# Kernel optimization log

Hardware: AMD Instinct MI355X
Metric: run time of the kernel (lower is better)

## Reference

```python
import jax, jax.numpy as jnp
import numpy as np

B, D, O = 16384, 1024, 1024
NUM_TASKS = 2
E = 4  # experts per group (2 task groups + 1 shared group)


def setup_inputs() -> dict:
    key = jax.random.key(0)
    ks = jax.random.split(key, 7)
    x = jax.random.normal(ks[0], (B, D), dtype=jnp.float32)
    # Stacked expert params: groups g in {task0, task1, shared}, each with E experts.
    W = jax.random.normal(ks[1], (3, E, D, O), dtype=jnp.float32) * 0.02  # Linear weight (in,out layout)
    b = jax.random.normal(ks[2], (3, E, O), dtype=jnp.float32) * 0.02
    # Per-task gates over (E specific + E shared) = 8 experts.
    Wg = jax.random.normal(ks[3], (NUM_TASKS, D, 2 * E), dtype=jnp.float32) * 0.02
    bg = jax.random.normal(ks[4], (NUM_TASKS, 2 * E), dtype=jnp.float32) * 0.02
    # Shared gate over all 3*E = 12 experts (is_top=False).
    Wgs = jax.random.normal(ks[5], (D, 3 * E), dtype=jnp.float32) * 0.02
    bgs = jax.random.normal(ks[6], (3 * E,), dtype=jnp.float32) * 0.02
    return {"x": x, "W": W, "b": b, "Wg": Wg, "bg": bg, "Wgs": Wgs, "bgs": bgs}


def reference(x, W, b, Wg, bg, Wgs, bgs):
    # All 12 experts share the same input (single-input branch): one batched GEMM.
    # h: [3, B, E, O]  (dropout is identity in eval mode)
    h = jax.nn.relu(jnp.einsum('bd,gedo->gbeo', x, W) + b[:, None, :, :])
    # Per-task gates: [T, B, 2E]
    sel_t = jax.nn.softmax(jnp.einsum('bd,tdm->tbm', x, Wg) + bg[:, None, :], axis=-1)
    outs = []
    for t in range(NUM_TASKS):
        mat = jnp.concatenate([h[t], h[2]], axis=1)  # [B, 2E, O]
        outs.append(jnp.einsum('bmo,bm->bo', mat, sel_t[t]))
    # Shared gate over all experts (is_top=False): [B, 3E]
    sel_s = jax.nn.softmax(x @ Wgs + bgs, axis=-1)
    mat_all = jnp.concatenate([h[0], h[1], h[2]], axis=1)  # [B, 3E, O]
    outs.append(jnp.einsum('bmo,bm->bo', mat_all, sel_s))
    return tuple(outs)
```

## Files before the change

### kernel.cpp

```cpp
#include <hip/hip_runtime.h>

typedef unsigned short ushort_t;
typedef __attribute__((ext_vector_type(8))) short short8;
typedef __attribute__((ext_vector_type(4))) float floatx4;

#define B_ROWS 16384
#define BO 16777216
#define MC 4096

__device__ __forceinline__ ushort_t f2bf(float f){
  unsigned u = __float_as_uint(f);
  u += 0x7fffu + ((u >> 16) & 1u);
  return (ushort_t)(u >> 16);
}
__device__ __forceinline__ float bf2f(ushort_t u){
  return __uint_as_float(((unsigned)u) << 16);
}

__device__ __forceinline__ void gld_lds16(void* l, const void* g){
  __builtin_amdgcn_global_load_lds(
      (__attribute__((address_space(1))) void*)(g),
      (__attribute__((address_space(3))) void*)(l), 16, 0, 0);
}

__global__ void cvt_x(const float* __restrict__ x, ushort_t* __restrict__ xb){
  const int i = (blockIdx.x * 256 + threadIdx.x) * 4;
  const floatx4 v = *(const floatx4*)(x + i);
  ushort4 o;
  o.x = f2bf(v[0]); o.y = f2bf(v[1]); o.z = f2bf(v[2]); o.w = f2bf(v[3]);
  *(ushort4*)(xb + i) = o;
}

__global__ void cvt_wt(const float* __restrict__ W, ushort_t* __restrict__ wt){
  __shared__ float t[64][65];
  const int blk = blockIdx.x;
  const int ge = blk >> 8, dt = (blk >> 4) & 15, ot = blk & 15;
  const float* src = W + ((size_t)ge << 20) + (size_t)(dt * 64) * 1024 + ot * 64;
  const int c4 = (threadIdx.x & 15) * 4, r0 = threadIdx.x >> 4;
#pragma unroll
  for (int p = 0; p < 4; ++p){
    const int r = r0 + p * 16;
    const floatx4 v = *(const floatx4*)(src + (size_t)r * 1024 + c4);
    t[r][c4] = v[0]; t[r][c4+1] = v[1]; t[r][c4+2] = v[2]; t[r][c4+3] = v[3];
  }
  __syncthreads();
  ushort_t* dst = wt + ((size_t)ge << 20) + (size_t)(ot * 64) * 1024 + dt * 64;
  const int d4 = (threadIdx.x & 15) * 4, o0 = threadIdx.x >> 4;
#pragma unroll
  for (int p = 0; p < 4; ++p){
    const int o = o0 + p * 16;
    ushort4 ov;
    ov.x = f2bf(t[d4][o]);   ov.y = f2bf(t[d4+1][o]);
    ov.z = f2bf(t[d4+2][o]); ov.w = f2bf(t[d4+3][o]);
    *(ushort4*)(dst + (size_t)o * 1024 + d4) = ov;
  }
}

__global__ void cvt_wg(const float* __restrict__ Wg, const float* __restrict__ bg,
                       const float* __restrict__ Wgs, const float* __restrict__ bgs,
                       ushort_t* __restrict__ wgcat, float* __restrict__ biascat){
  const int m = blockIdx.x;
#pragma unroll
  for (int j = 0; j < 4; ++j){
    const int d = j * 256 + threadIdx.x;
    float v;
    if (m < 16)      v = Wg[((size_t)((m >> 3) * 1024 + d)) * 8 + (m & 7)];
    else if (m < 28) v = Wgs[(size_t)d * 12 + (m - 16)];
    else             v = 0.f;
    wgcat[m * 1024 + d] = f2bf(v);
  }
  if (threadIdx.x == 0){
    float bv;
    if (m < 16)      bv = bg[m];
    else if (m < 28) bv = bgs[m - 16];
    else             bv = -1e30f;
    biascat[m] = bv;
  }
}

__global__ __launch_bounds__(256) void gates_mfma(
    const ushort_t* __restrict__ xb, const ushort_t* __restrict__ wgcat,
    const float* __restrict__ biascat, float* __restrict__ selT)
{
  __shared__ __align__(16) char gsm[20480];
  const int tid = threadIdx.x;
  const int lane = tid & 63;
  const int w = tid >> 6;
  const int lr = lane & 15;
  const int brow = blockIdx.x * 128;

  const int sc = (((tid & 7) ^ ((tid >> 3) & 7)) << 4);
  const char* aS = (const char*)xb + (size_t)(brow + (tid >> 3)) * 2048 + sc;
  const char* bS = (const char*)wgcat + (size_t)(tid >> 3) * 2048 + sc;

  const int kx0 = (((lane >> 4) << 4)) ^ ((lane & 7) << 4);
  const int kx1 = (64 + ((lane >> 4) << 4)) ^ ((lane & 7) << 4);

  int aOff[2], bOff[2];
#pragma unroll
  for (int m = 0; m < 2; ++m) aOff[m] = (w * 32 + m * 16 + lr) * 128;
#pragma unroll
  for (int n = 0; n < 2; ++n) bOff[n] = 16384 + (n * 16 + lr) * 128;

  const floatx4 fz = {0.f, 0.f, 0.f, 0.f};
  floatx4 hacc[2][2];
#pragma unroll
  for (int m = 0; m < 2; ++m)
#pragma unroll
    for (int n = 0; n < 2; ++n) hacc[m][n] = fz;

  for (int kt = 0; kt < 16; ++kt){
    const size_t ko = (size_t)kt * 128;
#pragma unroll
    for (int j = 0; j < 4; ++j)
      gld_lds16(gsm + j * 4096 + w * 1024, aS + (size_t)j * 65536 + ko);
    gld_lds16(gsm + 16384 + w * 1024, bS + ko);
    __syncthreads();
    short8 av[2][2], bv[2][2];
#pragma unroll
    for (int m = 0; m < 2; ++m){
      av[m][0] = *(const short8*)(gsm + aOff[m] + kx0);
      av[m][1] = *(const short8*)(gsm + aOff[m] + kx1);
    }
#pragma unroll
    for (int n = 0; n < 2; ++n){
      bv[n][0] = *(const short8*)(gsm + bOff[n] + kx0);
      bv[n][1] = *(const short8*)(gsm + bOff[n] + kx1);
    }
#pragma unroll
    for (int m = 0; m < 2; ++m)
#pragma unroll
      for (int n = 0; n < 2; ++n){
        hacc[m][n] = __builtin_amdgcn_mfma_f32_16x16x32_bf16(av[m][0], bv[n][0], hacc[m][n], 0, 0, 0);
        hacc[m][n] = __builtin_amdgcn_mfma_f32_16x16x32_bf16(av[m][1], bv[n][1], hacc[m][n], 0, 0, 0);
      }
    __syncthreads();
  }

  const float bc0 = biascat[lr];
  const float bc1 = biascat[16 + lr];
#pragma unroll
  for (int m = 0; m < 2; ++m){
#pragma unroll
    for (int r = 0; r < 4; ++r){
      float l0 = hacc[m][0][r] + bc0;
      float l1 = hacc[m][1][r] + bc1;
      float mx0 = l0;
#pragma unroll
      for (int s = 1; s < 8; s <<= 1) mx0 = fmaxf(mx0, __shfl_xor(mx0, s, 64));
      float e0 = __expf(l0 - mx0);
      float s0 = e0;
#pragma unroll
      for (int s = 1; s < 8; s <<= 1) s0 += __shfl_xor(s0, s, 64);
      float mx1 = l1;
#pragma unroll
      for (int s = 1; s < 16; s <<= 1) mx1 = fmaxf(mx1, __shfl_xor(mx1, s, 64));
      float e1 = __expf(l1 - mx1);
      float s1 = e1;
#pragma unroll
      for (int s = 1; s < 16; s <<= 1) s1 += __shfl_xor(s1, s, 64);
      const int row = brow + w * 32 + m * 16 + ((lane >> 4) << 2) + r;
      selT[(size_t)lr * B_ROWS + row] = e0 / s0;
      if (lr < 12) selT[(size_t)(16 + lr) * B_ROWS + row] = e1 / s1;
    }
  }
}

__global__ __launch_bounds__(512, 2) void pass1_gemm(
    const ushort_t* __restrict__ xb,
    const ushort_t* __restrict__ wt,
    const float* __restrict__ bias,
    ushort_t* __restrict__ h,
    int chunk_row0)
{
  __shared__ __align__(16) char smem[131072];
  const int tid  = threadIdx.x;
  const int lane = tid & 63;
  const int wv   = tid >> 6;
  const int wm   = wv >> 2;
  const int wn   = wv & 3;
  const int lr   = lane & 15;
  const int NT   = 48;

  const int bid = blockIdx.x;
  const int L = (bid & 7) * 32 + (bid >> 3);
  const int eg = L >> 6;
  const int nt = (L >> 4) & 3;
  const int mt = L & 15;
  const int brow_l = mt * 256;
  const int browg  = chunk_row0 + brow_l;
  const int bcol   = nt * 256;

  const int sc = (((tid & 7) ^ ((tid >> 3) & 7)) << 4);
  const char* aSrc[2];
  size_t bOffBase[2];
#pragma unroll
  for (int hh = 0; hh < 2; ++hh){
    aSrc[hh] = (const char*)xb + (size_t)(browg + hh * 128 + (tid >> 3)) * 2048 + sc;
    bOffBase[hh] = (size_t)(bcol + hh * 128 + (tid >> 3)) * 2048 + sc;
  }

  auto stageA = [&](int hh, int kt, int bo){
    char* d = smem + bo + hh * 16384 + wv * 1024;
    const char* s = aSrc[hh] + (size_t)(kt & 15) * 128;
    gld_lds16(d, s);
    gld_lds16(d + 8192, s + 131072);
  };
  auto stageB = [&](int hh, int kt, int bo){
    const int exk = eg * 3 + (kt >> 4);
    char* d = smem + bo + 32768 + hh * 16384 + wv * 1024;
    const char* s = (const char*)wt + ((size_t)exk << 21) + bOffBase[hh]
                  + (size_t)(kt & 15) * 128;
    gld_lds16(d, s);
    gld_lds16(d + 8192, s + 131072);
  };

  const int kx0 = (((lane >> 4) << 4)) ^ ((lane & 7) << 4);
  const int kx1 = (64 + ((lane >> 4) << 4)) ^ ((lane & 7) << 4);
  int aOff[8], bOff[4];
#pragma unroll
  for (int m = 0; m < 8; ++m) aOff[m] = wm * 16384 + (m * 16 + lr) * 128;
#pragma unroll
  for (int n = 0; n < 4; ++n)
    bOff[n] = 32768 + (wn >> 1) * 16384 + ((wn & 1) * 64 + n * 16 + lr) * 128;

  const floatx4 fz = {0.f, 0.f, 0.f, 0.f};
  floatx4 hacc[8][4];
#pragma unroll
  for (int m = 0; m < 8; ++m)
#pragma unroll
    for (int n = 0; n < 4; ++n) hacc[m][n] = fz;

  const int colb = bcol + wn * 64 + lr;
  float bi[3][4];
#pragma unroll
  for (int ee = 0; ee < 3; ++ee)
#pragma unroll
    for (int n = 0; n < 4; ++n)
      bi[ee][n] = bias[(eg * 3 + ee) * 1024 + colb + n * 16];

  auto EPI = [&](int el){
    ushort_t* hbase = h + ((size_t)(eg * 3 + el) * MC) * 1024;
#pragma unroll
    for (int m = 0; m < 8; ++m){
#pragma unroll
      for (int r = 0; r < 4; ++r){
        const int row = brow_l + wm * 128 + m * 16 + ((lane >> 4) << 2) + r;
        ushort_t* hp = hbase + (size_t)row * 1024 + colb;
#pragma unroll
        for (int n = 0; n < 4; ++n){
          float v = hacc[m][n][r] + bi[el][n];
          hp[n * 16] = f2bf(fmaxf(v, 0.f));
          hacc[m][n][r] = 0.f;
        }
      }
    }
  };

  stageA(0, 0, 0); stageA(1, 0, 0); stageB(0, 0, 0); stageB(1, 0, 0);
  stageB(0, 1, 65536); stageA(0, 1, 65536); stageA(1, 1, 65536);
  asm volatile("s_waitcnt vmcnt(6)" ::: "memory");
  __builtin_amdgcn_s_barrier();

#define LDF(X) (*(const short8*)(smem + (X)))
#define MFMA_(A, Bv, C) __builtin_amdgcn_mfma_f32_16x16x32_bf16(A, Bv, C, 0, 0, 0)
#define LGKM0_SB() { asm volatile("s_waitcnt lgkmcnt(0)" ::: "memory"); __builtin_amdgcn_sched_barrier(0); }

  for (int i = 0; i < NT; ++i){
    const int cur = (i & 1) << 16;
    const int nxt = cur ^ 65536;

    short8 a0[4][2], b0[2][2];
#pragma unroll
    for (int m = 0; m < 4; ++m){
      a0[m][0] = LDF(cur + aOff[m] + kx0);
      a0[m][1] = LDF(cur + aOff[m] + kx1);
    }
#pragma unroll
    for (int n = 0; n < 2; ++n){
      b0[n][0] = LDF(cur + bOff[n] + kx0);
      b0[n][1] = LDF(cur + bOff[n] + kx1);
    }
    if (i + 1 < NT) stageB(1, i + 1, nxt);
    __builtin_amdgcn_s_barrier();
    LGKM0_SB();
    __builtin_amdgcn_s_setprio(1);
#pragma unroll
    for (int m = 0; m < 4; ++m)
#pragma unroll
      for (int n = 0; n < 2; ++n){
        hacc[m][n] = MFMA_(a0[m][0], b0[n][0], hacc[m][n]);
        hacc[m][n] = MFMA_(a0[m][1], b0[n][1], hacc[m][n]);
      }
    __builtin_amdgcn_s_setprio(0);
    __builtin_amdgcn_s_barrier();

    short8 b1[2][2];
#pragma unroll
    for (int n = 0; n < 2; ++n){
      b1[n][0] = LDF(cur + bOff[2 + n] + kx0);
      b1[n][1] = LDF(cur + bOff[2 + n] + kx1);
    }
    __builtin_amdgcn_s_barrier();
    LGKM0_SB();
    __builtin_amdgcn_s_setprio(1);
#pragma unroll
    for (int m = 0; m < 4; ++m)
#pragma unroll
      for (int n = 0; n < 2; ++n){
        hacc[m][2 + n] = MFMA_(a0[m][0], b1[n][0], hacc[m][2 + n]);
        hacc[m][2 + n] = MFMA_(a0[m][1], b1[n][1], hacc[m][2 + n]);
      }
    __builtin_amdgcn_s_setprio(0);
    __builtin_amdgcn_s_barrier();

    short8 a1[4][2];
#pragma unroll
    for (int m = 0; m < 4; ++m){
      a1[m][0] = LDF(cur + aOff[4 + m] + kx0);
      a1[m][1] = LDF(cur + aOff[4 + m] + kx1);
    }
    if (i + 2 < NT) stageB(0, i + 2, cur);
    __builtin_amdgcn_s_barrier();
    LGKM0_SB();
    __builtin_amdgcn_s_setprio(1);
#pragma unroll
    for (int m = 0; m < 4; ++m)
#pragma unroll
      for (int n = 0; n < 2; ++n){
        hacc[4 + m][n] = MFMA_(a1[m][0], b0[n][0], hacc[4 + m][n]);
        hacc[4 + m][n] = MFMA_(a1[m][1], b0[n][1], hacc[4 + m][n]);
      }
    __builtin_amdgcn_s_setprio(0);
    __builtin_amdgcn_s_barrier();

    if (i + 2 < NT) { stageA(0, i + 2, cur); stageA(1, i + 2, cur); }
    __builtin_amdgcn_s_barrier();
    __builtin_amdgcn_s_setprio(1);
#pragma unroll
    for (int m = 0; m < 4; ++m)
#pragma unroll
      for (int n = 0; n < 2; ++n){
        hacc[4 + m][2 + n] = MFMA_(a1[m][0], b1[n][0], hacc[4 + m][2 + n]);
        hacc[4 + m][2 + n] = MFMA_(a1[m][1], b1[n][1], hacc[4 + m][2 + n]);
      }
    __builtin_amdgcn_s_setprio(0);
    if ((i & 15) == 15) EPI(i >> 4);
    if (i < NT - 2)       { asm volatile("s_waitcnt vmcnt(6)" ::: "memory"); }
    else if (i == NT - 2) { asm volatile("s_waitcnt vmcnt(0)" ::: "memory"); }
    __builtin_amdgcn_s_barrier();
  }
#undef LDF
#undef MFMA_
#undef LGKM0_SB
}

__global__ __launch_bounds__(256) void combine_kernel(
    const ushort_t* __restrict__ h,
    const float* __restrict__ selT,
    float* __restrict__ out,
    int row0)
{
  const int tid = threadIdx.x;
  const int lb  = blockIdx.x * 2 + (tid >> 7);
  const int b   = row0 + lb;
  const int c   = (tid & 127) * 8;
  const ushort_t* hp = h + (size_t)lb * 1024 + c;

  float a0[8], a1[8], as_[8];
#pragma unroll
  for (int k = 0; k < 8; ++k){ a0[k] = 0.f; a1[k] = 0.f; as_[k] = 0.f; }

#pragma unroll
  for (int e = 0; e < 4; ++e){
    const float w0 = selT[(size_t)e * B_ROWS + b];
    const float ws = selT[(size_t)(16 + e) * B_ROWS + b];
    const short8 hv = *(const short8*)(hp + (size_t)e * (MC * 1024));
#pragma unroll
    for (int k = 0; k < 8; ++k){
      const float f = bf2f((ushort_t)hv[k]);
      a0[k] += w0 * f; as_[k] += ws * f;
    }
  }
#pragma unroll
  for (int e = 0; e < 4; ++e){
    const float w1 = selT[(size_t)(8 + e) * B_ROWS + b];
    const float ws = selT[(size_t)(20 + e) * B_ROWS + b];
    const short8 hv = *(const short8*)(hp + (size_t)(4 + e) * (MC * 1024));
#pragma unroll
    for (int k = 0; k < 8; ++k){
      const float f = bf2f((ushort_t)hv[k]);
      a1[k] += w1 * f; as_[k] += ws * f;
    }
  }
#pragma unroll
  for (int e = 0; e < 4; ++e){
    const float w0 = selT[(size_t)(4 + e) * B_ROWS + b];
    const float w1 = selT[(size_t)(12 + e) * B_ROWS + b];
    const float ws = selT[(size_t)(24 + e) * B_ROWS + b];
    const short8 hv = *(const short8*)(hp + (size_t)(8 + e) * (MC * 1024));
#pragma unroll
    for (int k = 0; k < 8; ++k){
      const float f = bf2f((ushort_t)hv[k]);
      a0[k] += w0 * f; a1[k] += w1 * f; as_[k] += ws * f;
    }
  }

  float* o0 = out + (size_t)b * 1024 + c;
  *(floatx4*)(o0)     = *(const floatx4*)(a0);
  *(floatx4*)(o0 + 4) = *(const floatx4*)(a0 + 4);
  float* o1 = o0 + BO;
  *(floatx4*)(o1)     = *(const floatx4*)(a1);
  *(floatx4*)(o1 + 4) = *(const floatx4*)(a1 + 4);
  float* o2 = o1 + BO;
  *(floatx4*)(o2)     = *(const floatx4*)(as_);
  *(floatx4*)(o2 + 4) = *(const floatx4*)(as_ + 4);
}

__global__ void gates_kernel(const float* __restrict__ x,
                             const float* __restrict__ Wg,
                             const float* __restrict__ bg,
                             const float* __restrict__ Wgs,
                             const float* __restrict__ bgs,
                             float* __restrict__ selT)
{
  const int lane = threadIdx.x & 63;
  const int w    = threadIdx.x >> 6;
  const int b    = blockIdx.x * 4 + w;
  const float* xr = x + (size_t)b * 1024;
  float acc[28];
#pragma unroll
  for (int m = 0; m < 28; ++m) acc[m] = 0.f;
#pragma unroll
  for (int j = 0; j < 4; ++j){
    const int d0 = (j * 64 + lane) * 4;
    const floatx4 xv = *(const floatx4*)(xr + d0);
#pragma unroll
    for (int q = 0; q < 4; ++q){
      const float xs = xv[q];
      const int d = d0 + q;
      const float* g0 = Wg + d * 8;
      const float* g1 = Wg + 8192 + d * 8;
      const float* gs = Wgs + d * 12;
#pragma unroll
      for (int m = 0; m < 8; ++m)  acc[m]      += xs * g0[m];
#pragma unroll
      for (int m = 0; m < 8; ++m)  acc[8 + m]  += xs * g1[m];
#pragma unroll
      for (int m = 0; m < 12; ++m) acc[16 + m] += xs * gs[m];
    }
  }
#pragma unroll
  for (int m = 0; m < 28; ++m){
    float v = acc[m];
#pragma unroll
    for (int off = 1; off < 64; off <<= 1) v += __shfl_xor(v, off, 64);
    acc[m] = v;
  }
  if (lane == 0){
    float e0[8], e1[8], es[12];
    float mx0 = -1e30f, mx1 = -1e30f, mxs = -1e30f;
#pragma unroll
    for (int m = 0; m < 8; ++m){  e0[m] = acc[m]      + bg[m];     mx0 = fmaxf(mx0, e0[m]); }
#pragma unroll
    for (int m = 0; m < 8; ++m){  e1[m] = acc[8 + m]  + bg[8 + m]; mx1 = fmaxf(mx1, e1[m]); }
#pragma unroll
    for (int m = 0; m < 12; ++m){ es[m] = acc[16 + m] + bgs[m];    mxs = fmaxf(mxs, es[m]); }
    float s0 = 0.f, s1 = 0.f, ss = 0.f;
#pragma unroll
    for (int m = 0; m < 8; ++m){  e0[m] = __expf(e0[m] - mx0); s0 += e0[m]; }
#pragma unroll
    for (int m = 0; m < 8; ++m){  e1[m] = __expf(e1[m] - mx1); s1 += e1[m]; }
#pragma unroll
    for (int m = 0; m < 12; ++m){ es[m] = __expf(es[m] - mxs); ss += es[m]; }
    const float r0 = 1.f / s0, r1 = 1.f / s1, rs = 1.f / ss;
#pragma unroll
    for (int m = 0; m < 8; ++m)  selT[(size_t)m * B_ROWS + b]        = e0[m] * r0;
#pragma unroll
    for (int m = 0; m < 8; ++m)  selT[(size_t)(8 + m) * B_ROWS + b]  = e1[m] * r1;
#pragma unroll
    for (int m = 0; m < 12; ++m) selT[(size_t)(16 + m) * B_ROWS + b] = es[m] * rs;
  }
}

__global__ __launch_bounds__(256, 2) void moe_kernel(
    const ushort_t* __restrict__ xb,
    const ushort_t* __restrict__ wt,
    const float* __restrict__ bias,
    const float* __restrict__ selT,
    float* __restrict__ out)
{
  __shared__ __align__(16) char smem[24576];
  const int tid  = threadIdx.x;
  const int lane = tid & 63;
  const int wid  = tid >> 6;
  const int wm   = wid >> 1;
  const int wn   = wid & 1;
  const int brow = (blockIdx.x >> 4) << 7;
  const int bcol = (blockIdx.x & 15) << 6;
  const int rstg = tid >> 3;
  const int scol = ((tid & 7) << 4) ^ ((rstg & 7) << 4);
  size_t aoff[4], boff[2];
#pragma unroll
  for (int i = 0; i < 4; ++i) aoff[i] = (size_t)(brow + i * 32 + rstg) * 2048 + scol;
#pragma unroll
  for (int i = 0; i < 2; ++i) boff[i] = (size_t)(bcol + i * 32 + rstg) * 2048 + scol;
  char* aldst = smem + wid * 1024;
  char* bldst = smem + 16384 + wid * 1024;
  const int kl   = (lane >> 4) << 4;
  const int swzr = (lane & 7) << 4;
  int arow[4], brw[2];
#pragma unroll
  for (int m = 0; m < 4; ++m) arow[m] = (wm * 64 + m * 16 + (lane & 15)) * 128;
#pragma unroll
  for (int n = 0; n < 2; ++n) brw[n] = 16384 + (wn * 32 + n * 16 + (lane & 15)) * 128;
  const floatx4 fz = {0.f, 0.f, 0.f, 0.f};
  floatx4 o0a[4][2], o1a[4][2], osa[4][2];
#pragma unroll
  for (int m = 0; m < 4; ++m)
#pragma unroll
    for (int n = 0; n < 2; ++n){ o0a[m][n] = fz; o1a[m][n] = fz; osa[m][n] = fz; }
  const int c0 = bcol + wn * 32 + (lane & 15);
  const int rb = brow + wm * 64 + ((lane >> 4) << 2);
  for (int ex = 0; ex < 12; ++ex){
    floatx4 hacc[4][2];
#pragma unroll
    for (int m = 0; m < 4; ++m)
#pragma unroll
      for (int n = 0; n < 2; ++n) hacc[m][n] = fz;
    const size_t wbase = (size_t)ex << 21;
    for (int kt = 0; kt < 16; ++kt){
      const size_t ko = (size_t)kt << 7;
#pragma unroll
      for (int i = 0; i < 4; ++i)
        gld_lds16(aldst + i * 4096, (const char*)xb + aoff[i] + ko);
#pragma unroll
      for (int i = 0; i < 2; ++i)
        gld_lds16(bldst + i * 4096, (const char*)wt + wbase + boff[i] + ko);
      __syncthreads();
#pragma unroll
      for (int kk = 0; kk < 2; ++kk){
        short8 av[4], bv[2];
        const int kb = (kk << 6) + kl;
#pragma unroll
        for (int m = 0; m < 4; ++m)
          av[m] = *(const short8*)(smem + arow[m] + (kb ^ swzr));
#pragma unroll
        for (int n = 0; n < 2; ++n)
          bv[n] = *(const short8*)(smem + brw[n] + (kb ^ swzr));
#pragma unroll
        for (int m = 0; m < 4; ++m)
#pragma unroll
          for (int n = 0; n < 2; ++n)
            hacc[m][n] = __builtin_amdgcn_mfma_f32_16x16x32_bf16(av[m], bv[n], hacc[m][n], 0, 0, 0);
      }
      __syncthreads();
    }
    const int g = ex >> 2, e = ex & 3;
    const float bi0 = bias[ex * 1024 + c0];
    const float bi1 = bias[ex * 1024 + c0 + 16];
    int i0, i1, is_;
    if (g == 0)      { i0 = e;     i1 = -1;     is_ = 16 + e; }
    else if (g == 1) { i0 = -1;    i1 = 8 + e;  is_ = 20 + e; }
    else             { i0 = 4 + e; i1 = 12 + e; is_ = 24 + e; }
#pragma unroll
    for (int m = 0; m < 4; ++m){
      const int rg = rb + m * 16;
      const floatx4 wsv = *(const floatx4*)(selT + (size_t)is_ * B_ROWS + rg);
      floatx4 w0 = fz, w1 = fz;
      if (i0 >= 0) w0 = *(const floatx4*)(selT + (size_t)i0 * B_ROWS + rg);
      if (i1 >= 0) w1 = *(const floatx4*)(selT + (size_t)i1 * B_ROWS + rg);
#pragma unroll
      for (int n = 0; n < 2; ++n){
        const float bi = n ? bi1 : bi0;
#pragma unroll
        for (int r = 0; r < 4; ++r){
          float hv = hacc[m][n][r] + bi;
          hv = fmaxf(hv, 0.f);
          osa[m][n][r] += wsv[r] * hv;
          o0a[m][n][r] += w0[r] * hv;
          o1a[m][n][r] += w1[r] * hv;
        }
      }
    }
  }
#pragma unroll
  for (int m = 0; m < 4; ++m){
#pragma unroll
    for (int n = 0; n < 2; ++n){
#pragma unroll
      for (int r = 0; r < 4; ++r){
        const size_t idx = (size_t)(rb + m * 16 + r) * 1024 + (c0 + (n << 4));
        out[idx]          = o0a[m][n][r];
        out[idx + BO]     = o1a[m][n][r];
        out[idx + 2 * BO] = osa[m][n][r];
      }
    }
  }
}

extern "C" void kernel_launch(void* const* d_in, const int* in_sizes, int n_in,
                              void* d_out, int out_size, void* d_ws, size_t ws_size,
                              hipStream_t stream) {
  const float* x   = (const float*)d_in[0];
  const float* W   = (const float*)d_in[1];
  const float* b   = (const float*)d_in[2];
  const float* Wg  = (const float*)d_in[3];
  const float* bg  = (const float*)d_in[4];
  const float* Wgs = (const float*)d_in[5];
  const float* bgs = (const float*)d_in[6];
  float* out = (float*)d_out;

  char* ws = (char*)d_ws;
  ushort_t* xb   = (ushort_t*)ws;
  ushort_t* wtp  = (ushort_t*)(ws + 33554432);
  float*    selT = (float*)(ws + 58720256);
  ushort_t* wgc  = (ushort_t*)(ws + 60555264);
  float*    bcat = (float*)(ws + 60620800);
  ushort_t* hbuf = (ushort_t*)(ws + 67108864);

  const bool two_pass = ws_size >= (size_t)(67108864 + 12 * MC * 1024 * 2);

  cvt_x<<<dim3(16384), dim3(256), 0, stream>>>(x, xb);
  cvt_wt<<<dim3(3072), dim3(256), 0, stream>>>(W, wtp);

  if (two_pass){
    cvt_wg<<<dim3(32), dim3(256), 0, stream>>>(Wg, bg, Wgs, bgs, wgc, bcat);
    gates_mfma<<<dim3(128), dim3(256), 0, stream>>>(xb, wgc, bcat, selT);
    for (int c = 0; c < 16384 / MC; ++c){
      pass1_gemm<<<dim3(256), dim3(512), 0, stream>>>(xb, wtp, b, hbuf, c * MC);
      combine_kernel<<<dim3(MC / 2), dim3(256), 0, stream>>>(hbuf, selT, out, c * MC);
    }
  } else {
    gates_kernel<<<dim3(4096), dim3(256), 0, stream>>>(x, Wg, bg, Wgs, bgs, selT);
    moe_kernel<<<dim3(2048), dim3(256), 0, stream>>>(xb, wtp, b, selT, out);
  }
}
```

Baseline: 671.2 us.

## Switch expert GEMM to 32x32x16 MFMA with vectorized bias-relu epilogue

Replaces the 16x16x32 bf16 MFMA tiling with 32x32x16 MFMA tiles, restructuring the per-wave fragment loads, accumulators and swizzled LDS offsets. The larger instruction shape needs fewer LDS reads per FLOP and fewer MFMA issues. The epilogue now loads bias as float4 and writes packed 4-element bf16 stores. The vmcnt wait after the epilogue is relaxed to account for the extra outstanding stores. Operand order is swapped (B as the first operand) so the accumulator layout matches row-contiguous output stores.

```diff
diff --git a/kernel.cpp b/kernel.cpp
--- a/kernel.cpp
+++ b/kernel.cpp
@@ -3,6 +3,7 @@
 typedef unsigned short ushort_t;
 typedef __attribute__((ext_vector_type(8))) short short8;
 typedef __attribute__((ext_vector_type(4))) float floatx4;
+typedef __attribute__((ext_vector_type(16))) float floatx16;
 
 #define B_ROWS 16384
 #define BO 16777216
@@ -179,7 +180,8 @@
   const int wv   = tid >> 6;
   const int wm   = wv >> 2;
   const int wn   = wv & 3;
-  const int lr   = lane & 15;
+  const int l31  = lane & 31;
+  const int lhi  = lane >> 5;
   const int NT   = 48;
 
   const int bid = blockIdx.x;
@@ -215,43 +217,49 @@
     gld_lds16(d + 8192, s + 131072);
   };
 
-  const int kx0 = (((lane >> 4) << 4)) ^ ((lane & 7) << 4);
-  const int kx1 = (64 + ((lane >> 4) << 4)) ^ ((lane & 7) << 4);
-  int aOff[8], bOff[4];
-#pragma unroll
-  for (int m = 0; m < 8; ++m) aOff[m] = wm * 16384 + (m * 16 + lr) * 128;
-#pragma unroll
-  for (int n = 0; n < 4; ++n)
-    bOff[n] = 32768 + (wn >> 1) * 16384 + ((wn & 1) * 64 + n * 16 + lr) * 128;
-
-  const floatx4 fz = {0.f, 0.f, 0.f, 0.f};
-  floatx4 hacc[8][4];
-#pragma unroll
-  for (int m = 0; m < 8; ++m)
-#pragma unroll
-    for (int n = 0; n < 4; ++n) hacc[m][n] = fz;
-
-  const int colb = bcol + wn * 64 + lr;
-  float bi[3][4];
-#pragma unroll
-  for (int ee = 0; ee < 3; ++ee)
-#pragma unroll
-    for (int n = 0; n < 4; ++n)
-      bi[ee][n] = bias[(eg * 3 + ee) * 1024 + colb + n * 16];
-
+  const int swz = (lane & 7) << 4;
+  int kxv[4];
+#pragma unroll
+  for (int ks = 0; ks < 4; ++ks) kxv[ks] = (ks * 32 + lhi * 16) ^ swz;
+  int aO[4], bO[2];
+#pragma unroll
+  for (int mb = 0; mb < 4; ++mb) aO[mb] = wm * 16384 + (mb * 32 + l31) * 128;
+#pragma unroll
+  for (int nb = 0; nb < 2; ++nb)
+    bO[nb] = 32768 + (wn >> 1) * 16384 + ((wn & 1) * 64 + nb * 32 + l31) * 128;
+
+  floatx16 acc[4][2];
+#pragma unroll
+  for (int mb = 0; mb < 4; ++mb)
+#pragma unroll
+    for (int nb = 0; nb < 2; ++nb)
+#pragma unroll
+      for (int r = 0; r < 16; ++r) acc[mb][nb][r] = 0.f;
+
+  const int colw = bcol + wn * 64;
   auto EPI = [&](int el){
-    ushort_t* hbase = h + ((size_t)(eg * 3 + el) * MC) * 1024;
-#pragma unroll
-    for (int m = 0; m < 8; ++m){
-#pragma unroll
-      for (int r = 0; r < 4; ++r){
-        const int row = brow_l + wm * 128 + m * 16 + ((lane >> 4) << 2) + r;
-        ushort_t* hp = hbase + (size_t)row * 1024 + colb;
-#pragma unroll
-        for (int n = 0; n < 4; ++n){
-          float v = hacc[m][n][r] + bi[el][n];
-          hp[n * 16] = f2bf(fmaxf(v, 0.f));
-          hacc[m][n][r] = 0.f;
+    const int exk = eg * 3 + el;
+    ushort_t* hbase = h + ((size_t)exk * MC) * 1024;
+    const float* bb = bias + exk * 1024 + colw;
+#pragma unroll
+    for (int nb = 0; nb < 2; ++nb){
+#pragma unroll
+      for (int q = 0; q < 4; ++q){
+        const int cb = nb * 32 + q * 8 + lhi * 4;
+        const floatx4 bv = *(const floatx4*)(bb + cb);
+#pragma unroll
+        for (int mb = 0; mb < 4; ++mb){
+          const int row = brow_l + wm * 128 + mb * 32 + l31;
+          const float v0 = fmaxf(acc[mb][nb][4*q+0] + bv[0], 0.f);
+          const float v1 = fmaxf(acc[mb][nb][4*q+1] + bv[1], 0.f);
+          const float v2 = fmaxf(acc[mb][nb][4*q+2] + bv[2], 0.f);
+          const float v3 = fmaxf(acc[mb][nb][4*q+3] + bv[3], 0.f);
+          uint2 pk;
+          pk.x = (unsigned)f2bf(v0) | ((unsigned)f2bf(v1) << 16);
+          pk.y = (unsigned)f2bf(v2) | ((unsigned)f2bf(v3) << 16);
+          *(uint2*)(hbase + (size_t)row * 1024 + colw + cb) = pk;
+          acc[mb][nb][4*q+0] = 0.f; acc[mb][nb][4*q+1] = 0.f;
+          acc[mb][nb][4*q+2] = 0.f; acc[mb][nb][4*q+3] = 0.f;
         }
       }
     }
@@ -263,74 +271,64 @@
   __builtin_amdgcn_s_barrier();
 
 #define LDF(X) (*(const short8*)(smem + (X)))
-#define MFMA_(A, Bv, C) __builtin_amdgcn_mfma_f32_16x16x32_bf16(A, Bv, C, 0, 0, 0)
+#define MFMA32(A, Bv, C) __builtin_amdgcn_mfma_f32_32x32x16_bf16(A, Bv, C, 0, 0, 0)
 #define LGKM0_SB() { asm volatile("s_waitcnt lgkmcnt(0)" ::: "memory"); __builtin_amdgcn_sched_barrier(0); }
 
   for (int i = 0; i < NT; ++i){
     const int cur = (i & 1) << 16;
     const int nxt = cur ^ 65536;
 
-    short8 a0[4][2], b0[2][2];
-#pragma unroll
-    for (int m = 0; m < 4; ++m){
-      a0[m][0] = LDF(cur + aOff[m] + kx0);
-      a0[m][1] = LDF(cur + aOff[m] + kx1);
-    }
-#pragma unroll
-    for (int n = 0; n < 2; ++n){
-      b0[n][0] = LDF(cur + bOff[n] + kx0);
-      b0[n][1] = LDF(cur + bOff[n] + kx1);
-    }
+    short8 af[2][4], bf0[4];
+#pragma unroll
+    for (int mb = 0; mb < 2; ++mb)
+#pragma unroll
+      for (int ks = 0; ks < 4; ++ks)
+        af[mb][ks] = LDF(cur + aO[mb] + kxv[ks]);
+#pragma unroll
+    for (int ks = 0; ks < 4; ++ks)
+      bf0[ks] = LDF(cur + bO[0] + kxv[ks]);
     if (i + 1 < NT) stageB(1, i + 1, nxt);
     __builtin_amdgcn_s_barrier();
     LGKM0_SB();
     __builtin_amdgcn_s_setprio(1);
 #pragma unroll
-    for (int m = 0; m < 4; ++m)
-#pragma unroll
-      for (int n = 0; n < 2; ++n){
-        hacc[m][n] = MFMA_(a0[m][0], b0[n][0], hacc[m][n]);
-        hacc[m][n] = MFMA_(a0[m][1], b0[n][1], hacc[m][n]);
-      }
+    for (int mb = 0; mb < 2; ++mb)
+#pragma unroll
+      for (int ks = 0; ks < 4; ++ks)
+        acc[mb][0] = MFMA32(bf0[ks], af[mb][ks], acc[mb][0]);
     __builtin_amdgcn_s_setprio(0);
     __builtin_amdgcn_s_barrier();
 
-    short8 b1[2][2];
-#pragma unroll
-    for (int n = 0; n < 2; ++n){
-      b1[n][0] = LDF(cur + bOff[2 + n] + kx0);
-      b1[n][1] = LDF(cur + bOff[2 + n] + kx1);
-    }
+    short8 bf1[4];
+#pragma unroll
+    for (int ks = 0; ks < 4; ++ks)
+      bf1[ks] = LDF(cur + bO[1] + kxv[ks]);
     __builtin_amdgcn_s_barrier();
     LGKM0_SB();
     __builtin_amdgcn_s_setprio(1);
 #pragma unroll
-    for (int m = 0; m < 4; ++m)
-#pragma unroll
-      for (int n = 0; n < 2; ++n){
-        hacc[m][2 + n] = MFMA_(a0[m][0], b1[n][0], hacc[m][2 + n]);
-        hacc[m][2 + n] = MFMA_(a0[m][1], b1[n][1], hacc[m][2 + n]);
-      }
+    for (int mb = 0; mb < 2; ++mb)
+#pragma unroll
+      for (int ks = 0; ks < 4; ++ks)
+        acc[mb][1] = MFMA32(bf1[ks], af[mb][ks], acc[mb][1]);
     __builtin_amdgcn_s_setprio(0);
     __builtin_amdgcn_s_barrier();
 
-    short8 a1[4][2];
-#pragma unroll
-    for (int m = 0; m < 4; ++m){
-      a1[m][0] = LDF(cur + aOff[4 + m] + kx0);
-      a1[m][1] = LDF(cur + aOff[4 + m] + kx1);
-    }
+    short8 af2[2][4];
+#pragma unroll
+    for (int mb = 0; mb < 2; ++mb)
+#pragma unroll
+      for (int ks = 0; ks < 4; ++ks)
+        af2[mb][ks] = LDF(cur + aO[2 + mb] + kxv[ks]);
     if (i + 2 < NT) stageB(0, i + 2, cur);
     __builtin_amdgcn_s_barrier();
     LGKM0_SB();
     __builtin_amdgcn_s_setprio(1);
 #pragma unroll
-    for (int m = 0; m < 4; ++m)
-#pragma unroll
-      for (int n = 0; n < 2; ++n){
-        hacc[4 + m][n] = MFMA_(a1[m][0], b0[n][0], hacc[4 + m][n]);
-        hacc[4 + m][n] = MFMA_(a1[m][1], b0[n][1], hacc[4 + m][n]);
-      }
+    for (int mb = 0; mb < 2; ++mb)
+#pragma unroll
+      for (int ks = 0; ks < 4; ++ks)
+        acc[2 + mb][0] = MFMA32(bf0[ks], af2[mb][ks], acc[2 + mb][0]);
     __builtin_amdgcn_s_setprio(0);
     __builtin_amdgcn_s_barrier();
 
@@ -338,20 +336,19 @@
     __builtin_amdgcn_s_barrier();
     __builtin_amdgcn_s_setprio(1);
 #pragma unroll
-    for (int m = 0; m < 4; ++m)
-#pragma unroll
-      for (int n = 0; n < 2; ++n){
-        hacc[4 + m][2 + n] = MFMA_(a1[m][0], b1[n][0], hacc[4 + m][2 + n]);
-        hacc[4 + m][2 + n] = MFMA_(a1[m][1], b1[n][1], hacc[4 + m][2 + n]);
-      }
+    for (int mb = 0; mb < 2; ++mb)
+#pragma unroll
+      for (int ks = 0; ks < 4; ++ks)
+        acc[2 + mb][1] = MFMA32(bf1[ks], af2[mb][ks], acc[2 + mb][1]);
     __builtin_amdgcn_s_setprio(0);
     if ((i & 15) == 15) EPI(i >> 4);
-    if (i < NT - 2)       { asm volatile("s_waitcnt vmcnt(6)" ::: "memory"); }
-    else if (i == NT - 2) { asm volatile("s_waitcnt vmcnt(0)" ::: "memory"); }
+    if ((i & 15) == 15 && i < NT - 2)      { asm volatile("s_waitcnt vmcnt(38)" ::: "memory"); }
+    else if (i < NT - 2)                   { asm volatile("s_waitcnt vmcnt(6)"  ::: "memory"); }
+    else if (i == NT - 2)                  { asm volatile("s_waitcnt vmcnt(0)"  ::: "memory"); }
     __builtin_amdgcn_s_barrier();
   }
 #undef LDF
-#undef MFMA_
+#undef MFMA32
 #undef LGKM0_SB
 }
 
```

After: 741.7 us. 10.5% more time.
